# Kernel tuning notes

Measured on AMD Instinct MI355X. Metric: run time of the kernel, lower is better.

The kernel has to match this reference:

```python
import jax, jax.numpy as jnp
import numpy as np

B, S, D, H = 2, 2048, 1024, 16
HD = D // H  # head dim


def approx_gelu(x):
    return x * jax.nn.sigmoid(1.702 * x)


def setup_inputs() -> dict:
    key = jax.random.key(0)
    ks = jax.random.split(key, 12)
    q = jax.random.normal(ks[0], (B, S, D), jnp.float32)
    k = jax.random.normal(ks[1], (B, S, D), jnp.float32)
    v = jax.random.normal(ks[2], (B, S, D), jnp.float32)
    mask = jnp.zeros((B, 1, S, S), jnp.float32)
    sc = 0.02
    Wq = jax.random.normal(ks[3], (H, D, HD), jnp.float32) * sc
    bq = jax.random.normal(ks[4], (H, HD), jnp.float32) * sc
    Wk = jax.random.normal(ks[5], (H, D, HD), jnp.float32) * sc
    bk = jax.random.normal(ks[6], (H, HD), jnp.float32) * sc
    Wv = jax.random.normal(ks[7], (H, D, HD), jnp.float32) * sc
    bv = jax.random.normal(ks[8], (H, HD), jnp.float32) * sc
    Wo = jax.random.normal(ks[9], (D, D), jnp.float32) * sc
    bo = jax.random.normal(ks[10], (D,), jnp.float32) * sc
    return {"q": q, "k": k, "v": v, "mask": mask, "Wq": Wq, "bq": bq,
            "Wk": Wk, "bk": bk, "Wv": Wv, "bv": bv, "Wo": Wo, "bo": bo}


def reference(q, k, v, mask, Wq, bq, Wk, bk, Wv, bv, Wo, bo):
    # Per-head Q/K/V dense (no activation on projections, matching source).
    qh = jnp.einsum('bsd,hde->bhse', q, Wq) + bq[None, :, None, :]  # [B,H,S,HD]
    kh = jnp.einsum('bsd,hde->bhse', k, Wk) + bk[None, :, None, :]
    vh = jnp.einsum('bsd,hde->bhse', v, Wv) + bv[None, :, None, :]
    scale = 1.0 / jnp.sqrt(jnp.asarray(HD, qh.dtype))
    logits = jnp.einsum('bhse,bhte->bhst', qh, kh) * scale + mask  # [B,H,S,S]
    attn = jax.nn.softmax(logits, axis=-1)
    heads = jnp.einsum('bhst,bhte->bhse', attn, vh)  # [B,H,S,HD]
    # concat heads -> [B,S,D]
    x = jnp.transpose(heads, (0, 2, 1, 3)).reshape(q.shape[0], q.shape[1], D)
    return approx_gelu(x @ Wo + bo)
```

## Files before the change

kernel.cpp:

```cpp
#include <hip/hip_runtime.h>
#include <stdint.h>


typedef __bf16 bf16x8 __attribute__((ext_vector_type(8)));
typedef __bf16 bf16x4 __attribute__((ext_vector_type(4)));
typedef float f32x4 __attribute__((ext_vector_type(4)));
typedef float f32x16 __attribute__((ext_vector_type(16)));
typedef unsigned u32x4 __attribute__((ext_vector_type(4)));

static constexpr float L2E  = 1.4426950408889634f;
static constexpr float QSCL = 0.18033688011112042f;
static constexpr float GELC = -2.4554669595930157f;

__device__ __forceinline__ void async_load16(const void* g, void* l) {
    __builtin_amdgcn_global_load_lds(
        (const __attribute__((address_space(1))) unsigned int*)(uintptr_t)g,
        (__attribute__((address_space(3))) unsigned int*)(unsigned int)(uintptr_t)l,
        16, 0, 0);
}

template <int ROWS>
__device__ __forceinline__ void stage_tile(const __bf16* g, int ld, __bf16* lds, int tid) {
#pragma unroll
    for (int r = 0; r < ROWS / 32; ++r) {
        int p = r * 4096 + tid * 16;
        int row = p >> 7;
        int kbp = p & 127;
        int kbl = kbp ^ ((row & 7) << 4);
        async_load16((const char*)(g + (size_t)row * ld) + kbl,
                     (char*)lds + (p & ~1023));
    }
}

__device__ __forceinline__ bf16x8 lds_frag(const __bf16* base, int row, int kb) {
    return *(const bf16x8*)((const char*)base + (row << 7) + (kb ^ ((row & 7) << 4)));
}

__device__ __forceinline__ unsigned cvtpk(float a, float b) {
    unsigned d;
    asm("v_cvt_pk_bf16_f32 %0, %1, %2" : "=v"(d) : "v"(a), "v"(b));
    return d;
}
__device__ __forceinline__ void pswap(unsigned& a, unsigned& b) {
    asm("v_permlane32_swap_b32 %0, %1" : "+v"(a), "+v"(b));
}


__global__ __launch_bounds__(256) void cvt3_kernel(const float* __restrict__ q,
                                                   const float* __restrict__ k,
                                                   const float* __restrict__ v,
                                                   __bf16* __restrict__ qb,
                                                   __bf16* __restrict__ kb,
                                                   __bf16* __restrict__ vb) {
    int z = blockIdx.y;
    const float* src = z == 0 ? q : (z == 1 ? k : v);
    __bf16* dst = z == 0 ? qb : (z == 1 ? kb : vb);
    int i = blockIdx.x * 256 + threadIdx.x;
    f32x4 val = ((const f32x4*)src)[i];
    bf16x4 o;
    o[0] = (__bf16)val[0]; o[1] = (__bf16)val[1];
    o[2] = (__bf16)val[2]; o[3] = (__bf16)val[3];
    ((bf16x4*)dst)[i] = o;
}

__global__ __launch_bounds__(256) void mask_flags(const float* __restrict__ m,
                                                  unsigned* __restrict__ flags) {
    int i = blockIdx.x * 256 + threadIdx.x;
    f32x4 v = ((const f32x4*)m)[i];
    bool nz = (v[0] != 0.f) | (v[1] != 0.f) | (v[2] != 0.f) | (v[3] != 0.f);
    if (nz) {
        size_t i4 = (size_t)i * 4;
        int b = (int)(i4 >> 22);
        int rem = (int)(i4 & 4194303);
        int qq = rem >> 11, kv = rem & 2047;
        atomicOr(flags + (b * 16 + (qq >> 7)) * 32 + (kv >> 6), 1u);
    }
}

__global__ __launch_bounds__(256) void pack_wqkv(const float* __restrict__ Wq,
                                                 const float* __restrict__ Wk,
                                                 const float* __restrict__ Wv,
                                                 __bf16* __restrict__ out) {
    __shared__ __bf16 T[64][72];
    int tid = threadIdx.x;
    int k0 = blockIdx.x * 64, h = blockIdx.y, z = blockIdx.z;
    const float* W = z == 0 ? Wq : (z == 1 ? Wk : Wv);
#pragma unroll
    for (int it = 0; it < 4; ++it) {
        int idx = it * 1024 + tid * 4;
        int r = idx >> 6, e = idx & 63;
        f32x4 val = *(const f32x4*)(W + ((size_t)h * 1024 + k0 + r) * 64 + e);
#pragma unroll
        for (int j = 0; j < 4; ++j) T[r][e + j] = (__bf16)val[j];
    }
    __syncthreads();
    int e2 = tid >> 2, kc = (tid & 3) * 16;
    bf16x8 o0, o1;
#pragma unroll
    for (int i = 0; i < 8; ++i) { o0[i] = T[kc + i][e2]; o1[i] = T[kc + 8 + i][e2]; }
    __bf16* dst = out + ((size_t)z << 20) + (size_t)(h * 64 + e2) * 1024 + k0 + kc;
    *(bf16x8*)dst = o0;
    *(bf16x8*)(dst + 8) = o1;
}

__global__ __launch_bounds__(256) void pack_wo(const float* __restrict__ Wo,
                                               __bf16* __restrict__ out) {
    __shared__ __bf16 T[64][72];
    int tid = threadIdx.x;
    int k0 = blockIdx.x * 64, n0 = blockIdx.y * 64;
#pragma unroll
    for (int it = 0; it < 4; ++it) {
        int idx = it * 1024 + tid * 4;
        int r = idx >> 6, e = idx & 63;
        f32x4 val = *(const f32x4*)(Wo + (size_t)(k0 + r) * 1024 + n0 + e);
#pragma unroll
        for (int j = 0; j < 4; ++j) T[r][e + j] = (__bf16)val[j];
    }
    __syncthreads();
    int e2 = tid >> 2, kc = (tid & 3) * 16;
    bf16x8 o0, o1;
#pragma unroll
    for (int i = 0; i < 8; ++i) { o0[i] = T[kc + i][e2]; o1[i] = T[kc + 8 + i][e2]; }
    __bf16* dst = out + (size_t)(n0 + e2) * 1024 + k0 + kc;
    *(bf16x8*)dst = o0;
    *(bf16x8*)(dst + 8) = o1;
}

__global__ __launch_bounds__(256) void gemm_qkv(
    const __bf16* __restrict__ qb, const __bf16* __restrict__ kb,
    const __bf16* __restrict__ vb, const __bf16* __restrict__ w3,
    const float* __restrict__ bq, const float* __restrict__ bk,
    const float* __restrict__ bv,
    __bf16* __restrict__ Qp, __bf16* __restrict__ Kp, __bf16* __restrict__ Vp) {
    __shared__ __bf16 As[128 * 64];
    __shared__ __bf16 Bs[128 * 64];
    int z = blockIdx.z;
    const __bf16* A = z == 0 ? qb : (z == 1 ? kb : vb);
    const __bf16* Bt = w3 + ((size_t)z << 20);
    const float* bias = z == 0 ? bq : (z == 1 ? bk : bv);
    float sc = z == 0 ? QSCL : 1.0f;

    int tid = threadIdx.x;
    int w = tid >> 6, lane = tid & 63, lg = lane >> 4, lr = lane & 15;
    int wr = (w >> 1) * 64, wc = (w & 1) * 64;
    int m0 = blockIdx.x * 128, n0 = blockIdx.y * 128;
    f32x4 acc[4][4] = {};
    for (int k0 = 0; k0 < 1024; k0 += 64) {
        __syncthreads();
        stage_tile<128>(A + (size_t)m0 * 1024 + k0, 1024, As, tid);
        stage_tile<128>(Bt + (size_t)n0 * 1024 + k0, 1024, Bs, tid);
        __syncthreads();
#pragma unroll
        for (int kk = 0; kk < 2; ++kk) {
            bf16x8 af[4], bfr[4];
#pragma unroll
            for (int t = 0; t < 4; ++t) {
                af[t] = lds_frag(As, wr + t * 16 + lr, lg * 16 + kk * 64);
                bfr[t] = lds_frag(Bs, wc + t * 16 + lr, lg * 16 + kk * 64);
            }
#pragma unroll
            for (int i = 0; i < 4; ++i)
#pragma unroll
                for (int j = 0; j < 4; ++j)
                    acc[i][j] = __builtin_amdgcn_mfma_f32_16x16x32_bf16(
                        af[i], bfr[j], acc[i][j], 0, 0, 0);
        }
    }
#pragma unroll
    for (int i = 0; i < 4; ++i) {
        int mb = m0 + wr + i * 16 + lg * 4;
        int b = mb >> 11, s = mb & 2047;
#pragma unroll
        for (int j = 0; j < 4; ++j) {
            int n = n0 + wc + j * 16 + lr;
            float bvv = bias[n];
            int h = n >> 6, e = n & 63;
            int bh = b * 16 + h;
            if (z == 2) {
                size_t addr = ((size_t)bh * 32 + (s >> 6)) * 4096 + (e >> 5) * 2048 +
                              ((s >> 4) & 3) * 512 + ((s >> 3) & 1) * 256 +
                              (e & 31) * 8 + (s & 7);
                bf16x4 o;
#pragma unroll
                for (int r = 0; r < 4; ++r) o[r] = (__bf16)(acc[i][j][r] + bvv);
                *(bf16x4*)(Vp + addr) = o;
            } else {
                __bf16* out = z == 0 ? Qp : Kp;
                size_t base = ((size_t)bh * 64 + (s >> 5)) * 2048 + (e >> 4) * 512 +
                              ((e >> 3) & 1) * 256 + (s & 31) * 8 + (e & 7);
#pragma unroll
                for (int r = 0; r < 4; ++r)
                    out[base + r * 8] = (__bf16)((acc[i][j][r] + bvv) * sc);
            }
        }
    }
}

__global__ __launch_bounds__(256) void gemm_out(const __bf16* __restrict__ A,
                                                const __bf16* __restrict__ Bt,
                                                const float* __restrict__ bias,
                                                float* __restrict__ dst) {
    __shared__ __bf16 As[64 * 64];
    __shared__ __bf16 Bs[128 * 64];
    int tid = threadIdx.x;
    int w = tid >> 6, lane = tid & 63, lg = lane >> 4, lr = lane & 15;
    int wr = (w >> 1) * 32, wc = (w & 1) * 64;
    int m0 = blockIdx.x * 64, n0 = blockIdx.y * 128;
    f32x4 acc[2][4] = {};
    for (int k0 = 0; k0 < 1024; k0 += 64) {
        __syncthreads();
        stage_tile<64>(A + (size_t)m0 * 1024 + k0, 1024, As, tid);
        stage_tile<128>(Bt + (size_t)n0 * 1024 + k0, 1024, Bs, tid);
        __syncthreads();
#pragma unroll
        for (int kk = 0; kk < 2; ++kk) {
            bf16x8 af[2], bfr[4];
#pragma unroll
            for (int t = 0; t < 2; ++t)
                af[t] = lds_frag(As, wr + t * 16 + lr, lg * 16 + kk * 64);
#pragma unroll
            for (int t = 0; t < 4; ++t)
                bfr[t] = lds_frag(Bs, wc + t * 16 + lr, lg * 16 + kk * 64);
#pragma unroll
            for (int i = 0; i < 2; ++i)
#pragma unroll
                for (int j = 0; j < 4; ++j)
                    acc[i][j] = __builtin_amdgcn_mfma_f32_16x16x32_bf16(
                        af[i], bfr[j], acc[i][j], 0, 0, 0);
        }
    }
#pragma unroll
    for (int i = 0; i < 2; ++i) {
        int mb = m0 + wr + i * 16 + lg * 4;
#pragma unroll
        for (int j = 0; j < 4; ++j) {
            int n = n0 + wc + j * 16 + lr;
            float bvv = bias[n];
#pragma unroll
            for (int r = 0; r < 4; ++r) {
                float v = acc[i][j][r] + bvv;
                float g = v / (1.f + exp2f(GELC * v));
                dst[(size_t)(mb + r) * 1024 + n] = g;
            }
        }
    }
}

__global__ __launch_bounds__(256) void attn_kernel(
    const __bf16* __restrict__ Qp, const __bf16* __restrict__ Kp,
    const __bf16* __restrict__ Vp, const float* __restrict__ mask,
    const unsigned* __restrict__ flags,
    __bf16* __restrict__ Op0, __bf16* __restrict__ Op1,
    float* __restrict__ lacc) {
    int tid = threadIdx.x;
    int w = tid >> 6, l = tid & 63;
    int q31 = l & 31, hi = l >> 5;
    int i = blockIdx.x;
    int xcd = i & 7, j = i >> 3;
    int group = (j >> 4) * 8 + xcd;
    int qt = j & 15;
    int bh = group & 31, z = group >> 5;
    int b = bh >> 4, h = bh & 15;
    int qw = qt * 128 + w * 32;

    const __bf16* Qb = Qp + ((size_t)bh * 64 + (qw >> 5)) * 2048 + l * 8;
    bf16x8 qf[4];
#pragma unroll
    for (int kk = 0; kk < 4; ++kk) qf[kk] = *(const bf16x8*)(Qb + kk * 512);

    const __bf16* Kb = Kp + ((size_t)bh * 64 + z * 32) * 2048 + l * 8;
    const __bf16* Vb = Vp + ((size_t)bh * 32 + z * 16) * 4096 + l * 8;
    const float* mrow = mask + (size_t)b * 4194304 + (size_t)(qw + q31) * 2048 + (z << 10) + hi * 4;
    const unsigned* flg = flags + (b * 16 + qt) * 32 + z * 16;

    f32x16 O[2] = {};
    float la0 = 0.f, la1 = 0.f;

    bf16x8 kf[2][4];
#pragma unroll
    for (int mt = 0; mt < 2; ++mt)
#pragma unroll
        for (int kk = 0; kk < 4; ++kk)
            kf[mt][kk] = *(const bf16x8*)(Kb + (mt * 4 + kk) * 512);

    for (int kt = 0; kt < 16; ++kt) {
        f32x16 T[2] = {};
        __builtin_amdgcn_s_setprio(1);
#pragma unroll
        for (int kk = 0; kk < 4; ++kk)
#pragma unroll
            for (int mt = 0; mt < 2; ++mt)
                T[mt] = __builtin_amdgcn_mfma_f32_32x32x16_bf16(kf[mt][kk], qf[kk], T[mt], 0, 0, 0);
        __builtin_amdgcn_s_setprio(0);

        bf16x8 vf[2][4];
#pragma unroll
        for (int mt = 0; mt < 2; ++mt)
#pragma unroll
            for (int kk = 0; kk < 4; ++kk)
                vf[mt][kk] = *(const bf16x8*)(Vb + (size_t)kt * 4096 + (mt * 4 + kk) * 512);
        if (kt < 15) {
#pragma unroll
            for (int mt = 0; mt < 2; ++mt)
#pragma unroll
                for (int kk = 0; kk < 4; ++kk)
                    kf[mt][kk] = *(const bf16x8*)(Kb + ((size_t)(kt + 1) * 2 + mt) * 2048 + kk * 512);
        }

        unsigned fl = __builtin_amdgcn_readfirstlane(flg[kt]);
        if (fl) {
#pragma unroll
            for (int mt = 0; mt < 2; ++mt)
#pragma unroll
                for (int g = 0; g < 4; ++g) {
                    f32x4 mk = *(const f32x4*)(mrow + kt * 64 + mt * 32 + g * 8);
#pragma unroll
                    for (int c = 0; c < 4; ++c)
                        T[mt][4 * g + c] = fmaf(mk[c], L2E, T[mt][4 * g + c]);
                }
        }
#pragma unroll
        for (int g = 0; g < 4; ++g) {
            float a0 = exp2f(T[0][4 * g + 0]);
            float a1 = exp2f(T[0][4 * g + 1]);
            float a2 = exp2f(T[0][4 * g + 2]);
            float a3 = exp2f(T[0][4 * g + 3]);
            float b0 = exp2f(T[1][4 * g + 0]);
            float b1 = exp2f(T[1][4 * g + 1]);
            float b2 = exp2f(T[1][4 * g + 2]);
            float b3 = exp2f(T[1][4 * g + 3]);
            la0 += (a0 + a1) + (a2 + a3);
            la1 += (b0 + b1) + (b2 + b3);
            T[0][4 * g + 0] = a0; T[0][4 * g + 1] = a1;
            T[0][4 * g + 2] = a2; T[0][4 * g + 3] = a3;
            T[1][4 * g + 0] = b0; T[1][4 * g + 1] = b1;
            T[1][4 * g + 2] = b2; T[1][4 * g + 3] = b3;
        }

        bf16x8 pf[4];
#pragma unroll
        for (int kk = 0; kk < 4; ++kk) {
            int mt = kk >> 1;
            int gA = (2 * kk) & 3, gB = gA + 1;
            unsigned x0 = cvtpk(T[mt][4 * gA + 0], T[mt][4 * gA + 1]);
            unsigned x1 = cvtpk(T[mt][4 * gA + 2], T[mt][4 * gA + 3]);
            unsigned y0 = cvtpk(T[mt][4 * gB + 0], T[mt][4 * gB + 1]);
            unsigned y1 = cvtpk(T[mt][4 * gB + 2], T[mt][4 * gB + 3]);
            pswap(x0, y0);
            pswap(x1, y1);
            u32x4 packed; packed[0] = x0; packed[1] = x1; packed[2] = y0; packed[3] = y1;
            pf[kk] = __builtin_bit_cast(bf16x8, packed);
        }

        __builtin_amdgcn_s_setprio(1);
#pragma unroll
        for (int kk = 0; kk < 4; ++kk)
#pragma unroll
            for (int mt = 0; mt < 2; ++mt)
                O[mt] = __builtin_amdgcn_mfma_f32_32x32x16_bf16(vf[mt][kk], pf[kk], O[mt], 0, 0, 0);
        __builtin_amdgcn_s_setprio(0);
    }

    float l_acc = la0 + la1;
    l_acc += __shfl_xor(l_acc, 32, 64);
    if (hi == 0)
        lacc[((size_t)z * 32 + b * 16 + h) * 2048 + qw + q31] = l_acc;
    __bf16* Ob = (z ? Op1 : Op0) + (((size_t)(b * 16 + h)) * 2048 + qw + q31) * 64 + hi * 4;
#pragma unroll
    for (int mt = 0; mt < 2; ++mt)
#pragma unroll
        for (int g = 0; g < 4; ++g) {
            bf16x4 o;
#pragma unroll
            for (int c = 0; c < 4; ++c) o[c] = (__bf16)O[mt][4 * g + c];
            *(bf16x4*)(Ob + mt * 32 + g * 8) = o;
        }
}

__global__ __launch_bounds__(256) void attn_norm(const __bf16* __restrict__ Op0,
                                                 const __bf16* __restrict__ Op1,
                                                 const float* __restrict__ lacc,
                                                 __bf16* __restrict__ x) {
    int idx = blockIdx.x * 256 + threadIdx.x;
    int b = idx >> 19;
    int rem = idx & 524287;
    int h = rem >> 15;
    int s = (rem >> 4) & 2047;
    int e0 = (rem & 15) * 4;
    size_t base = (((size_t)(b * 16 + h)) * 2048 + s) * 64 + e0;
    bf16x4 a = *(const bf16x4*)(Op0 + base);
    bf16x4 c = *(const bf16x4*)(Op1 + base);
    size_t li = ((size_t)(b * 16 + h)) * 2048 + s;
    float inv = 1.0f / (lacc[li] + lacc[65536 + li]);
    bf16x4 r;
#pragma unroll
    for (int j = 0; j < 4; ++j)
        r[j] = (__bf16)(((float)a[j] + (float)c[j]) * inv);
    *(bf16x4*)(x + ((size_t)b * 2048 + s) * 1024 + h * 64 + e0) = r;
}


extern "C" void kernel_launch(void* const* d_in, const int* in_sizes, int n_in,
                              void* d_out, int out_size, void* d_ws, size_t ws_size,
                              hipStream_t stream) {
    const float* q    = (const float*)d_in[0];
    const float* k    = (const float*)d_in[1];
    const float* v    = (const float*)d_in[2];
    const float* mask = (const float*)d_in[3];
    const float* Wq   = (const float*)d_in[4];
    const float* bq   = (const float*)d_in[5];
    const float* Wk   = (const float*)d_in[6];
    const float* bk   = (const float*)d_in[7];
    const float* Wv   = (const float*)d_in[8];
    const float* bv   = (const float*)d_in[9];
    const float* Wo   = (const float*)d_in[10];
    const float* bo   = (const float*)d_in[11];

    char* ws = (char*)d_ws;
    __bf16* qb  = (__bf16*)(ws + (0ull  << 20));
    __bf16* kb  = (__bf16*)(ws + (8ull  << 20));
    __bf16* vb  = (__bf16*)(ws + (16ull << 20));
    __bf16* w3  = (__bf16*)(ws + (24ull << 20));
    __bf16* wo  = (__bf16*)(ws + (30ull << 20));
    __bf16* Qpk = (__bf16*)(ws + (32ull << 20));
    __bf16* Kpk = (__bf16*)(ws + (40ull << 20));
    __bf16* Vpk = (__bf16*)(ws + (48ull << 20));
    float*  laccp = (float*)(ws + (56ull << 20));
    unsigned* flagp = (unsigned*)(ws + (56ull << 20) + (512ull << 10));
    __bf16* Op0 = qb;
    __bf16* Op1 = kb;
    __bf16* xp  = vb;

    cvt3_kernel<<<dim3(4096, 3), 256, 0, stream>>>(q, k, v, qb, kb, vb);
    pack_wqkv<<<dim3(16, 16, 3), 256, 0, stream>>>(Wq, Wk, Wv, w3);
    pack_wo<<<dim3(16, 16), 256, 0, stream>>>(Wo, wo);
    hipMemsetAsync(flagp, 0, 4096, stream);
    mask_flags<<<8192, 256, 0, stream>>>(mask, flagp);

    gemm_qkv<<<dim3(32, 8, 3), 256, 0, stream>>>(qb, kb, vb, w3, bq, bk, bv,
                                                 Qpk, Kpk, Vpk);

    attn_kernel<<<dim3(1024), 256, 0, stream>>>(Qpk, Kpk, Vpk, mask, flagp,
                                                Op0, Op1, laccp);
    attn_norm<<<4096, 256, 0, stream>>>(Op0, Op1, laccp, xp);

    gemm_out<<<dim3(64, 8), 256, 0, stream>>>(xp, wo, bo, (float*)d_out);
}
```

Measured before the change: 157.0 us.

## Fuse fp32-to-bf16 input conversion into QKV GEMM staging and merge weight packs

The separate cvt3 kernel, which converted q/k/v to bf16 in workspace, is removed. The QKV GEMM now loads fp32 activations directly, converts them with packed bf16 conversion and writes them into swizzled LDS. The two weight-packing kernels are also merged into one launch. This drops a full round trip of the activations through memory and two kernel launches. The cost is that each A tile, loaded 8 times across N blocks, is now read as fp32 at twice the bytes, and the synchronous global-to-register-to-LDS path replaces async global_load_lds.

New measurement: 161.4 us. 1.03x slower.

```diff
diff --git a/kernel.cpp b/kernel.cpp
--- a/kernel.cpp
+++ b/kernel.cpp
@@ -45,23 +45,24 @@
     asm("v_permlane32_swap_b32 %0, %1" : "+v"(a), "+v"(b));
 }
 
-
-__global__ __launch_bounds__(256) void cvt3_kernel(const float* __restrict__ q,
-                                                   const float* __restrict__ k,
-                                                   const float* __restrict__ v,
-                                                   __bf16* __restrict__ qb,
-                                                   __bf16* __restrict__ kb,
-                                                   __bf16* __restrict__ vb) {
-    int z = blockIdx.y;
-    const float* src = z == 0 ? q : (z == 1 ? k : v);
-    __bf16* dst = z == 0 ? qb : (z == 1 ? kb : vb);
-    int i = blockIdx.x * 256 + threadIdx.x;
-    f32x4 val = ((const f32x4*)src)[i];
-    bf16x4 o;
-    o[0] = (__bf16)val[0]; o[1] = (__bf16)val[1];
-    o[2] = (__bf16)val[2]; o[3] = (__bf16)val[3];
-    ((bf16x4*)dst)[i] = o;
-}
+__device__ __forceinline__ void stage_a_f32(const float* g, __bf16* lds, int tid) {
+    int rsub = tid >> 3;
+    int c8 = (tid & 7) * 8;
+#pragma unroll
+    for (int pass = 0; pass < 4; ++pass) {
+        int row = pass * 32 + rsub;
+        const float* src = g + (size_t)row * 1024 + c8;
+        f32x4 a = *(const f32x4*)src;
+        f32x4 b = *(const f32x4*)(src + 4);
+        u32x4 pk;
+        pk[0] = cvtpk(a[0], a[1]);
+        pk[1] = cvtpk(a[2], a[3]);
+        pk[2] = cvtpk(b[0], b[1]);
+        pk[3] = cvtpk(b[2], b[3]);
+        *(u32x4*)((char*)lds + row * 128 + ((c8 * 2) ^ ((row & 7) << 4))) = pk;
+    }
+}
+
 
 __global__ __launch_bounds__(256) void mask_flags(const float* __restrict__ m,
                                                   unsigned* __restrict__ flags) {
@@ -77,65 +78,66 @@
     }
 }
 
-__global__ __launch_bounds__(256) void pack_wqkv(const float* __restrict__ Wq,
-                                                 const float* __restrict__ Wk,
-                                                 const float* __restrict__ Wv,
-                                                 __bf16* __restrict__ out) {
+__global__ __launch_bounds__(256) void pack_w4(const float* __restrict__ Wq,
+                                               const float* __restrict__ Wk,
+                                               const float* __restrict__ Wv,
+                                               const float* __restrict__ Wo,
+                                               __bf16* __restrict__ w3,
+                                               __bf16* __restrict__ wo) {
     __shared__ __bf16 T[64][72];
     int tid = threadIdx.x;
-    int k0 = blockIdx.x * 64, h = blockIdx.y, z = blockIdx.z;
-    const float* W = z == 0 ? Wq : (z == 1 ? Wk : Wv);
-#pragma unroll
-    for (int it = 0; it < 4; ++it) {
-        int idx = it * 1024 + tid * 4;
-        int r = idx >> 6, e = idx & 63;
-        f32x4 val = *(const f32x4*)(W + ((size_t)h * 1024 + k0 + r) * 64 + e);
-#pragma unroll
-        for (int j = 0; j < 4; ++j) T[r][e + j] = (__bf16)val[j];
-    }
-    __syncthreads();
-    int e2 = tid >> 2, kc = (tid & 3) * 16;
-    bf16x8 o0, o1;
-#pragma unroll
-    for (int i = 0; i < 8; ++i) { o0[i] = T[kc + i][e2]; o1[i] = T[kc + 8 + i][e2]; }
-    __bf16* dst = out + ((size_t)z << 20) + (size_t)(h * 64 + e2) * 1024 + k0 + kc;
-    *(bf16x8*)dst = o0;
-    *(bf16x8*)(dst + 8) = o1;
-}
-
-__global__ __launch_bounds__(256) void pack_wo(const float* __restrict__ Wo,
-                                               __bf16* __restrict__ out) {
-    __shared__ __bf16 T[64][72];
-    int tid = threadIdx.x;
-    int k0 = blockIdx.x * 64, n0 = blockIdx.y * 64;
-#pragma unroll
-    for (int it = 0; it < 4; ++it) {
-        int idx = it * 1024 + tid * 4;
-        int r = idx >> 6, e = idx & 63;
-        f32x4 val = *(const f32x4*)(Wo + (size_t)(k0 + r) * 1024 + n0 + e);
-#pragma unroll
-        for (int j = 0; j < 4; ++j) T[r][e + j] = (__bf16)val[j];
-    }
-    __syncthreads();
-    int e2 = tid >> 2, kc = (tid & 3) * 16;
-    bf16x8 o0, o1;
-#pragma unroll
-    for (int i = 0; i < 8; ++i) { o0[i] = T[kc + i][e2]; o1[i] = T[kc + 8 + i][e2]; }
-    __bf16* dst = out + (size_t)(n0 + e2) * 1024 + k0 + kc;
-    *(bf16x8*)dst = o0;
-    *(bf16x8*)(dst + 8) = o1;
+    int z = blockIdx.z;
+    int k0 = blockIdx.x * 64;
+    if (z < 3) {
+        int h = blockIdx.y;
+        const float* W = z == 0 ? Wq : (z == 1 ? Wk : Wv);
+#pragma unroll
+        for (int it = 0; it < 4; ++it) {
+            int idx = it * 1024 + tid * 4;
+            int r = idx >> 6, e = idx & 63;
+            f32x4 val = *(const f32x4*)(W + ((size_t)h * 1024 + k0 + r) * 64 + e);
+#pragma unroll
+            for (int j = 0; j < 4; ++j) T[r][e + j] = (__bf16)val[j];
+        }
+        __syncthreads();
+        int e2 = tid >> 2, kc = (tid & 3) * 16;
+        bf16x8 o0, o1;
+#pragma unroll
+        for (int i = 0; i < 8; ++i) { o0[i] = T[kc + i][e2]; o1[i] = T[kc + 8 + i][e2]; }
+        __bf16* dst = w3 + ((size_t)z << 20) + (size_t)(h * 64 + e2) * 1024 + k0 + kc;
+        *(bf16x8*)dst = o0;
+        *(bf16x8*)(dst + 8) = o1;
+    } else {
+        int n0 = blockIdx.y * 64;
+#pragma unroll
+        for (int it = 0; it < 4; ++it) {
+            int idx = it * 1024 + tid * 4;
+            int r = idx >> 6, e = idx & 63;
+            f32x4 val = *(const f32x4*)(Wo + (size_t)(k0 + r) * 1024 + n0 + e);
+#pragma unroll
+            for (int j = 0; j < 4; ++j) T[r][e + j] = (__bf16)val[j];
+        }
+        __syncthreads();
+        int e2 = tid >> 2, kc = (tid & 3) * 16;
+        bf16x8 o0, o1;
+#pragma unroll
+        for (int i = 0; i < 8; ++i) { o0[i] = T[kc + i][e2]; o1[i] = T[kc + 8 + i][e2]; }
+        __bf16* dst = wo + (size_t)(n0 + e2) * 1024 + k0 + kc;
+        *(bf16x8*)dst = o0;
+        *(bf16x8*)(dst + 8) = o1;
+    }
 }
 
 __global__ __launch_bounds__(256) void gemm_qkv(
-    const __bf16* __restrict__ qb, const __bf16* __restrict__ kb,
-    const __bf16* __restrict__ vb, const __bf16* __restrict__ w3,
+    const float* __restrict__ qf32, const float* __restrict__ kf32,
+    const float* __restrict__ vf32, const __bf16* __restrict__ w3,
     const float* __restrict__ bq, const float* __restrict__ bk,
     const float* __restrict__ bv,
     __bf16* __restrict__ Qp, __bf16* __restrict__ Kp, __bf16* __restrict__ Vp) {
     __shared__ __bf16 As[128 * 64];
     __shared__ __bf16 Bs[128 * 64];
     int z = blockIdx.z;
-    const __bf16* A = z == 0 ? qb : (z == 1 ? kb : vb);
+    const float* A = z == 0 ? qf32 : (z == 1 ? kf32 : vf32);
     const __bf16* Bt = w3 + ((size_t)z << 20);
     const float* bias = z == 0 ? bq : (z == 1 ? bk : bv);
     float sc = z == 0 ? QSCL : 1.0f;
@@ -147,7 +149,7 @@
     f32x4 acc[4][4] = {};
     for (int k0 = 0; k0 < 1024; k0 += 64) {
         __syncthreads();
-        stage_tile<128>(A + (size_t)m0 * 1024 + k0, 1024, As, tid);
+        stage_a_f32(A + (size_t)m0 * 1024 + k0, As, tid);
         stage_tile<128>(Bt + (size_t)n0 * 1024 + k0, 1024, Bs, tid);
         __syncthreads();
 #pragma unroll
@@ -417,9 +419,9 @@
     const float* bo   = (const float*)d_in[11];
 
     char* ws = (char*)d_ws;
-    __bf16* qb  = (__bf16*)(ws + (0ull  << 20));
-    __bf16* kb  = (__bf16*)(ws + (8ull  << 20));
-    __bf16* vb  = (__bf16*)(ws + (16ull << 20));
+    __bf16* Op0 = (__bf16*)(ws + (0ull  << 20));
+    __bf16* Op1 = (__bf16*)(ws + (8ull  << 20));
+    __bf16* xp  = (__bf16*)(ws + (16ull << 20));
     __bf16* w3  = (__bf16*)(ws + (24ull << 20));
     __bf16* wo  = (__bf16*)(ws + (30ull << 20));
     __bf16* Qpk = (__bf16*)(ws + (32ull << 20));
@@ -427,17 +429,12 @@
     __bf16* Vpk = (__bf16*)(ws + (48ull << 20));
     float*  laccp = (float*)(ws + (56ull << 20));
     unsigned* flagp = (unsigned*)(ws + (56ull << 20) + (512ull << 10));
-    __bf16* Op0 = qb;
-    __bf16* Op1 = kb;
-    __bf16* xp  = vb;
-
-    cvt3_kernel<<<dim3(4096, 3), 256, 0, stream>>>(q, k, v, qb, kb, vb);
-    pack_wqkv<<<dim3(16, 16, 3), 256, 0, stream>>>(Wq, Wk, Wv, w3);
-    pack_wo<<<dim3(16, 16), 256, 0, stream>>>(Wo, wo);
+
+    pack_w4<<<dim3(16, 16, 4), 256, 0, stream>>>(Wq, Wk, Wv, Wo, w3, wo);
     hipMemsetAsync(flagp, 0, 4096, stream);
     mask_flags<<<8192, 256, 0, stream>>>(mask, flagp);
 
-    gemm_qkv<<<dim3(32, 8, 3), 256, 0, stream>>>(qb, kb, vb, w3, bq, bk, bv,
+    gemm_qkv<<<dim3(32, 8, 3), 256, 0, stream>>>(q, k, v, w3, bq, bk, bv,
                                                  Qpk, Kpk, Vpk);
 
     attn_kernel<<<dim3(1024), 256, 0, stream>>>(Qpk, Kpk, Vpk, mask, flagp,
```

## Stage K/V tiles in LDS via async double-buffering and merge weight packing kernels

Applied to the files above, without the earlier changes.

The attention kernel previously had each wave load K and V fragments directly from global memory into registers. It now loads each K/V tile once per block into double-buffered shared memory using global_load_lds, prefetching the next tile while the current one is consumed. This cuts redundant global/L2 traffic across the four waves, at the cost of a __syncthreads per iteration and added LDS reads. Separately, the Wqkv and Wo packing kernels are merged into one launch to save a kernel launch.

Result: no change. 158.1 us (+0.7%).

```diff
diff --git a/kernel.cpp b/kernel.cpp
--- a/kernel.cpp
+++ b/kernel.cpp
@@ -77,53 +77,54 @@
     }
 }
 
-__global__ __launch_bounds__(256) void pack_wqkv(const float* __restrict__ Wq,
-                                                 const float* __restrict__ Wk,
-                                                 const float* __restrict__ Wv,
-                                                 __bf16* __restrict__ out) {
+__global__ __launch_bounds__(256) void pack_w4(const float* __restrict__ Wq,
+                                               const float* __restrict__ Wk,
+                                               const float* __restrict__ Wv,
+                                               const float* __restrict__ Wo,
+                                               __bf16* __restrict__ w3,
+                                               __bf16* __restrict__ wo) {
     __shared__ __bf16 T[64][72];
     int tid = threadIdx.x;
-    int k0 = blockIdx.x * 64, h = blockIdx.y, z = blockIdx.z;
-    const float* W = z == 0 ? Wq : (z == 1 ? Wk : Wv);
-#pragma unroll
-    for (int it = 0; it < 4; ++it) {
-        int idx = it * 1024 + tid * 4;
-        int r = idx >> 6, e = idx & 63;
-        f32x4 val = *(const f32x4*)(W + ((size_t)h * 1024 + k0 + r) * 64 + e);
-#pragma unroll
-        for (int j = 0; j < 4; ++j) T[r][e + j] = (__bf16)val[j];
-    }
-    __syncthreads();
-    int e2 = tid >> 2, kc = (tid & 3) * 16;
-    bf16x8 o0, o1;
-#pragma unroll
-    for (int i = 0; i < 8; ++i) { o0[i] = T[kc + i][e2]; o1[i] = T[kc + 8 + i][e2]; }
-    __bf16* dst = out + ((size_t)z << 20) + (size_t)(h * 64 + e2) * 1024 + k0 + kc;
-    *(bf16x8*)dst = o0;
-    *(bf16x8*)(dst + 8) = o1;
-}
-
-__global__ __launch_bounds__(256) void pack_wo(const float* __restrict__ Wo,
-                                               __bf16* __restrict__ out) {
-    __shared__ __bf16 T[64][72];
-    int tid = threadIdx.x;
-    int k0 = blockIdx.x * 64, n0 = blockIdx.y * 64;
-#pragma unroll
-    for (int it = 0; it < 4; ++it) {
-        int idx = it * 1024 + tid * 4;
-        int r = idx >> 6, e = idx & 63;
-        f32x4 val = *(const f32x4*)(Wo + (size_t)(k0 + r) * 1024 + n0 + e);
-#pragma unroll
-        for (int j = 0; j < 4; ++j) T[r][e + j] = (__bf16)val[j];
-    }
-    __syncthreads();
-    int e2 = tid >> 2, kc = (tid & 3) * 16;
-    bf16x8 o0, o1;
-#pragma unroll
-    for (int i = 0; i < 8; ++i) { o0[i] = T[kc + i][e2]; o1[i] = T[kc + 8 + i][e2]; }
-    __bf16* dst = out + (size_t)(n0 + e2) * 1024 + k0 + kc;
-    *(bf16x8*)dst = o0;
-    *(bf16x8*)(dst + 8) = o1;
+    int z = blockIdx.z;
+    int k0 = blockIdx.x * 64;
+    if (z < 3) {
+        int h = blockIdx.y;
+        const float* W = z == 0 ? Wq : (z == 1 ? Wk : Wv);
+#pragma unroll
+        for (int it = 0; it < 4; ++it) {
+            int idx = it * 1024 + tid * 4;
+            int r = idx >> 6, e = idx & 63;
+            f32x4 val = *(const f32x4*)(W + ((size_t)h * 1024 + k0 + r) * 64 + e);
+#pragma unroll
+            for (int j = 0; j < 4; ++j) T[r][e + j] = (__bf16)val[j];
+        }
+        __syncthreads();
+        int e2 = tid >> 2, kc = (tid & 3) * 16;
+        bf16x8 o0, o1;
+#pragma unroll
+        for (int i = 0; i < 8; ++i) { o0[i] = T[kc + i][e2]; o1[i] = T[kc + 8 + i][e2]; }
+        __bf16* dst = w3 + ((size_t)z << 20) + (size_t)(h * 64 + e2) * 1024 + k0 + kc;
+        *(bf16x8*)dst = o0;
+        *(bf16x8*)(dst + 8) = o1;
+    } else {
+        int n0 = blockIdx.y * 64;
+#pragma unroll
+        for (int it = 0; it < 4; ++it) {
+            int idx = it * 1024 + tid * 4;
+            int r = idx >> 6, e = idx & 63;
+            f32x4 val = *(const f32x4*)(Wo + (size_t)(k0 + r) * 1024 + n0 + e);
+#pragma unroll
+            for (int j = 0; j < 4; ++j) T[r][e + j] = (__bf16)val[j];
+        }
+        __syncthreads();
+        int e2 = tid >> 2, kc = (tid & 3) * 16;
+        bf16x8 o0, o1;
+#pragma unroll
+        for (int i = 0; i < 8; ++i) { o0[i] = T[kc + i][e2]; o1[i] = T[kc + 8 + i][e2]; }
+        __bf16* dst = wo + (size_t)(n0 + e2) * 1024 + k0 + kc;
+        *(bf16x8*)dst = o0;
+        *(bf16x8*)(dst + 8) = o1;
+    }
 }
 
 __global__ __launch_bounds__(256) void gemm_qkv(
@@ -252,6 +253,8 @@
     const unsigned* __restrict__ flags,
     __bf16* __restrict__ Op0, __bf16* __restrict__ Op1,
     float* __restrict__ lacc) {
+    __shared__ __bf16 Ks[2][4096];
+    __shared__ __bf16 Vs[2][4096];
     int tid = threadIdx.x;
     int w = tid >> 6, l = tid & 63;
     int q31 = l & 31, hi = l >> 5;
@@ -268,44 +271,44 @@
 #pragma unroll
     for (int kk = 0; kk < 4; ++kk) qf[kk] = *(const bf16x8*)(Qb + kk * 512);
 
-    const __bf16* Kb = Kp + ((size_t)bh * 64 + z * 32) * 2048 + l * 8;
-    const __bf16* Vb = Vp + ((size_t)bh * 32 + z * 16) * 4096 + l * 8;
+    const __bf16* Kb = Kp + ((size_t)bh * 64 + z * 32) * 2048;
+    const __bf16* Vb = Vp + ((size_t)bh * 32 + z * 16) * 4096;
     const float* mrow = mask + (size_t)b * 4194304 + (size_t)(qw + q31) * 2048 + (z << 10) + hi * 4;
     const unsigned* flg = flags + (b * 16 + qt) * 32 + z * 16;
 
     f32x16 O[2] = {};
     float la0 = 0.f, la1 = 0.f;
 
-    bf16x8 kf[2][4];
-#pragma unroll
-    for (int mt = 0; mt < 2; ++mt)
-#pragma unroll
-        for (int kk = 0; kk < 4; ++kk)
-            kf[mt][kk] = *(const bf16x8*)(Kb + (mt * 4 + kk) * 512);
+#pragma unroll
+    for (int r = 0; r < 2; ++r) {
+        int p = r * 4096 + tid * 16;
+        async_load16((const char*)Kb + p, (char*)Ks[0] + (p & ~1023));
+        async_load16((const char*)Vb + p, (char*)Vs[0] + (p & ~1023));
+    }
 
     for (int kt = 0; kt < 16; ++kt) {
+        int buf = kt & 1;
+        __syncthreads();
+        if (kt < 15) {
+#pragma unroll
+            for (int r = 0; r < 2; ++r) {
+                int p = r * 4096 + tid * 16;
+                async_load16((const char*)(Kb + (size_t)(kt + 1) * 4096) + p,
+                             (char*)Ks[buf ^ 1] + (p & ~1023));
+                async_load16((const char*)(Vb + (size_t)(kt + 1) * 4096) + p,
+                             (char*)Vs[buf ^ 1] + (p & ~1023));
+            }
+        }
         f32x16 T[2] = {};
         __builtin_amdgcn_s_setprio(1);
 #pragma unroll
         for (int kk = 0; kk < 4; ++kk)
 #pragma unroll
-            for (int mt = 0; mt < 2; ++mt)
-                T[mt] = __builtin_amdgcn_mfma_f32_32x32x16_bf16(kf[mt][kk], qf[kk], T[mt], 0, 0, 0);
+            for (int mt = 0; mt < 2; ++mt) {
+                bf16x8 a = *(const bf16x8*)(Ks[buf] + mt * 2048 + kk * 512 + l * 8);
+                T[mt] = __builtin_amdgcn_mfma_f32_32x32x16_bf16(a, qf[kk], T[mt], 0, 0, 0);
+            }
         __builtin_amdgcn_s_setprio(0);
-
-        bf16x8 vf[2][4];
-#pragma unroll
-        for (int mt = 0; mt < 2; ++mt)
-#pragma unroll
-            for (int kk = 0; kk < 4; ++kk)
-                vf[mt][kk] = *(const bf16x8*)(Vb + (size_t)kt * 4096 + (mt * 4 + kk) * 512);
-        if (kt < 15) {
-#pragma unroll
-            for (int mt = 0; mt < 2; ++mt)
-#pragma unroll
-                for (int kk = 0; kk < 4; ++kk)
-                    kf[mt][kk] = *(const bf16x8*)(Kb + ((size_t)(kt + 1) * 2 + mt) * 2048 + kk * 512);
-        }
 
         unsigned fl = __builtin_amdgcn_readfirstlane(flg[kt]);
         if (fl) {
@@ -356,8 +359,10 @@
 #pragma unroll
         for (int kk = 0; kk < 4; ++kk)
 #pragma unroll
-            for (int mt = 0; mt < 2; ++mt)
-                O[mt] = __builtin_amdgcn_mfma_f32_32x32x16_bf16(vf[mt][kk], pf[kk], O[mt], 0, 0, 0);
+            for (int mt = 0; mt < 2; ++mt) {
+                bf16x8 vv = *(const bf16x8*)(Vs[buf] + mt * 2048 + kk * 512 + l * 8);
+                O[mt] = __builtin_amdgcn_mfma_f32_32x32x16_bf16(vv, pf[kk], O[mt], 0, 0, 0);
+            }
         __builtin_amdgcn_s_setprio(0);
     }
 
@@ -432,8 +437,7 @@
     __bf16* xp  = vb;
 
     cvt3_kernel<<<dim3(4096, 3), 256, 0, stream>>>(q, k, v, qb, kb, vb);
-    pack_wqkv<<<dim3(16, 16, 3), 256, 0, stream>>>(Wq, Wk, Wv, w3);
-    pack_wo<<<dim3(16, 16), 256, 0, stream>>>(Wo, wo);
+    pack_w4<<<dim3(16, 16, 4), 256, 0, stream>>>(Wq, Wk, Wv, Wo, w3, wo);
     hipMemsetAsync(flagp, 0, 4096, stream);
     mask_flags<<<8192, 256, 0, stream>>>(mask, flagp);
 
```
